# Performance work log

Hardware: AMD Instinct MI355X
Metric: run time of the kernel (lower is better)

Reference implementation:

```python
import jax, jax.numpy as jnp
import numpy as np

N_HEADS = 16
HEAD_DIM = 64
HIDDEN = N_HEADS * HEAD_DIM


def setup_inputs() -> dict:
    key = jax.random.key(0)
    ks = jax.random.split(key, 10)
    B, F, T = 2, 2048, 2048
    std = 0.02
    inp = {
        "from_tensor": jax.random.normal(ks[0], (B, F, HIDDEN), dtype=jnp.float32),
        "to_tensor": jax.random.normal(ks[1], (B, T, HIDDEN), dtype=jnp.float32),
        "attention_mask": jax.random.randint(ks[2], (B, F, T), 0, 2, dtype=jnp.int32),
        "Wq": jax.random.normal(ks[3], (HIDDEN, HIDDEN), dtype=jnp.float32) * std,
        "bq": jnp.zeros((HIDDEN,), dtype=jnp.float32),
        "Wk": jax.random.normal(ks[4], (HIDDEN, HIDDEN), dtype=jnp.float32) * std,
        "bk": jnp.zeros((HIDDEN,), dtype=jnp.float32),
        "Wv": jax.random.normal(ks[5], (HIDDEN, HIDDEN), dtype=jnp.float32) * std,
        "bv": jnp.zeros((HIDDEN,), dtype=jnp.float32),
    }
    return inp


def reference(from_tensor, to_tensor, attention_mask, Wq, bq, Wk, bk, Wv, bv):
    B, F, _ = from_tensor.shape
    T = to_tensor.shape[1]
    N, H = N_HEADS, HEAD_DIM

    # QKV projections (no activations: query/key/value act fns are None)
    q = (from_tensor @ Wq + bq).reshape(B, F, N, H)
    k = (to_tensor @ Wk + bk).reshape(B, T, N, H)
    v = (to_tensor @ Wv + bv).reshape(B, T, N, H)

    scores = jnp.einsum('BFNH,BTNH->BNFT', q, k) * (1.0 / np.sqrt(float(H)))
    # additive mask: mask [B,F,T] -> [B,1,F,T]; 0 entries get -10000
    adder = (1.0 - attention_mask.astype(jnp.float32))[:, None, :, :] * -10000.0
    scores = scores + adder
    probs = jax.nn.softmax(scores, axis=-1)  # dropout skipped (inference)

    context = jnp.einsum('BNFT,BTNH->BFNH', probs, v)
    return context.reshape(B, F, N * H)
```

## Files before the change

### kernel.cpp

```cpp
#include <hip/hip_runtime.h>


typedef short v8s __attribute__((ext_vector_type(8)));
typedef float v4f __attribute__((ext_vector_type(4)));
typedef unsigned short u16;
typedef unsigned int   u32;
typedef unsigned long long u64;

constexpr float QSCALE = 0.18033688011112042f;

__device__ __forceinline__ u16 f2bf(float f) {
    u32 u = __builtin_bit_cast(u32, f);
    u += 0x7fffu + ((u >> 16) & 1u);
    return (u16)(u >> 16);
}

__device__ __forceinline__ u32 pack_trunc(float a, float b) {
    return __builtin_amdgcn_perm(__builtin_bit_cast(u32, b),
                                 __builtin_bit_cast(u32, a), 0x07060302u);
}

__device__ __forceinline__ v8s ld8(const u16* p) {
    return *reinterpret_cast<const v8s*>(p);
}

__device__ __forceinline__ void async16(const void* g, void* l) {
    __builtin_amdgcn_global_load_lds(
        (const __attribute__((address_space(1))) u32*)g,
        (__attribute__((address_space(3))) u32*)l, 16, 0, 0);
}

__global__ __launch_bounds__(256) void prep(
    const float* __restrict__ from, const float* __restrict__ to,
    u16* __restrict__ Xf, u16* __restrict__ Xt,
    const float* __restrict__ Wq, const float* __restrict__ Wk, const float* __restrict__ Wv,
    u16* __restrict__ Wqt, u16* __restrict__ Wkt, u16* __restrict__ Wvt,
    const int* __restrict__ mask, u64* __restrict__ words) {
    __shared__ float tile[32][33];
    const int bid = blockIdx.x, tid = threadIdx.x;
    if (bid < 8192) {
        int i = bid * 256 + tid;
        const float4* s;
        ushort4* d;
        int j;
        if (i < 1048576) { s = (const float4*)from; d = (ushort4*)Xf; j = i; }
        else             { s = (const float4*)to;   d = (ushort4*)Xt; j = i - 1048576; }
        float4 v = s[j];
        ushort4 o;
        o.x = f2bf(v.x); o.y = f2bf(v.y); o.z = f2bf(v.z); o.w = f2bf(v.w);
        d[j] = o;
    } else if (bid < 11264) {
        const int r = bid - 8192;
        const int zz = r >> 10, rem = r & 1023;
        const float* W = zz == 0 ? Wq : (zz == 1 ? Wk : Wv);
        u16* Wt = zz == 0 ? Wqt : (zz == 1 ? Wkt : Wvt);
        const int tx = tid & 31, ty = tid >> 5;
        const int n0 = (rem & 31) * 32, k0 = (rem >> 5) * 32;
        for (int i = 0; i < 4; i++)
            tile[ty + i * 8][tx] = W[(size_t)(k0 + ty + i * 8) * 1024 + n0 + tx];
        __syncthreads();
        for (int i = 0; i < 4; i++)
            Wt[(size_t)(n0 + ty + i * 8) * 1024 + k0 + tx] = f2bf(tile[tx][ty + i * 8]);
    } else {
        int g = (bid - 11264) * 256 + tid;
        int w = g >> 6, lane = g & 63;
        int v = mask[(size_t)w * 64 + lane];
        u64 bits = __ballot(v != 0);
        if (lane == 0) words[w] = bits;
    }
}

__global__ __launch_bounds__(256) void gemm_qkv(
    const u16* __restrict__ Xf, const u16* __restrict__ Xt,
    const u16* __restrict__ Wqt, const u16* __restrict__ Wkt, const u16* __restrict__ Wvt,
    const float* __restrict__ bq, const float* __restrict__ bk, const float* __restrict__ bv,
    u16* __restrict__ Qb, u16* __restrict__ Kb, u16* __restrict__ Vtb) {
    const int z = blockIdx.z;
    const u16* A      = z == 0 ? Xf : Xt;
    const u16* Bt     = z == 0 ? Wqt : (z == 1 ? Wkt : Wvt);
    const float* bias = z == 0 ? bq : (z == 1 ? bk : bv);
    u16* C            = z == 0 ? Qb : (z == 1 ? Kb : Vtb);
    const int mode    = (z == 2);
    const float sc    = (z == 0) ? QSCALE : 1.0f;

    __shared__ u16 As[2][128][32];
    __shared__ u16 Bs[2][128][32];
    const uint4* Ag = reinterpret_cast<const uint4*>(A);
    const uint4* Bg = reinterpret_cast<const uint4*>(Bt);

    const int tid = threadIdx.x;
    const int lane = tid & 63, wave = tid >> 6;
    const int quad = lane >> 4, l16 = lane & 15;
    const int wm = wave >> 1, wn = wave & 1;
    const int m0 = blockIdx.x * 128, n0 = blockIdx.y * 128;

    const int cg  = (lane & 3) ^ ((lane >> 3) & 3);
    const int sw8 = (quad ^ ((l16 >> 1) & 3)) * 8;

    const int gi0 = wave * 4;
    const uint4 *ap0, *ap1, *ap2, *ap3, *bp0, *bp1, *bp2, *bp3;
    {
        const int rl = lane >> 2;
        const int rb0 = ((gi0 + 0) & 7) * 16 + rl, kh0 = (gi0 + 0) >> 3;
        const int rb1 = ((gi0 + 1) & 7) * 16 + rl, kh1 = (gi0 + 1) >> 3;
        const int rb2 = ((gi0 + 2) & 7) * 16 + rl, kh2 = (gi0 + 2) >> 3;
        const int rb3 = ((gi0 + 3) & 7) * 16 + rl, kh3 = (gi0 + 3) >> 3;
        ap0 = Ag + (size_t)(m0 + rb0) * 128 + kh0 * 4 + cg;
        ap1 = Ag + (size_t)(m0 + rb1) * 128 + kh1 * 4 + cg;
        ap2 = Ag + (size_t)(m0 + rb2) * 128 + kh2 * 4 + cg;
        ap3 = Ag + (size_t)(m0 + rb3) * 128 + kh3 * 4 + cg;
        bp0 = Bg + (size_t)(n0 + rb0) * 128 + kh0 * 4 + cg;
        bp1 = Bg + (size_t)(n0 + rb1) * 128 + kh1 * 4 + cg;
        bp2 = Bg + (size_t)(n0 + rb2) * 128 + kh2 * 4 + cg;
        bp3 = Bg + (size_t)(n0 + rb3) * 128 + kh3 * 4 + cg;
    }
    u16* Asl = (u16*)As + gi0 * 512;
    u16* Bsl = (u16*)Bs + gi0 * 512;

    v4f acc[4][4];
    for (int i = 0; i < 4; i++)
        for (int j = 0; j < 4; j++) acc[i][j] = (v4f)0.0f;

    for (int k0 = 0; k0 < 16; k0++) {
        __syncthreads();
        async16(ap0, Asl);        ap0 += 8;
        async16(ap1, Asl + 512);  ap1 += 8;
        async16(ap2, Asl + 1024); ap2 += 8;
        async16(ap3, Asl + 1536); ap3 += 8;
        async16(bp0, Bsl);        bp0 += 8;
        async16(bp1, Bsl + 512);  bp1 += 8;
        async16(bp2, Bsl + 1024); bp2 += 8;
        async16(bp3, Bsl + 1536); bp3 += 8;
        __syncthreads();

        #pragma unroll
        for (int kk = 0; kk < 2; kk++) {
            v8s af[4], bf[4];
            #pragma unroll
            for (int mt = 0; mt < 4; mt++) af[mt] = ld8(&As[kk][wm * 64 + mt * 16 + l16][sw8]);
            #pragma unroll
            for (int nt = 0; nt < 4; nt++) bf[nt] = ld8(&Bs[kk][wn * 64 + nt * 16 + l16][sw8]);
            #pragma unroll
            for (int mt = 0; mt < 4; mt++)
                #pragma unroll
                for (int nt = 0; nt < 4; nt++)
                    acc[mt][nt] = __builtin_amdgcn_mfma_f32_16x16x32_bf16(af[mt], bf[nt], acc[mt][nt], 0, 0, 0);
        }
    }

    #pragma unroll
    for (int nt = 0; nt < 4; nt++) {
        const int col = n0 + wn * 64 + nt * 16 + l16;
        const float bvv = bias[col];
        #pragma unroll
        for (int mt = 0; mt < 4; mt++) {
            const int mbase = m0 + wm * 64 + mt * 16 + quad * 4;
            if (mode == 0) {
                for (int r = 0; r < 4; r++)
                    C[(size_t)(mbase + r) * 1024 + col] = f2bf((acc[mt][nt][r] + bvv) * sc);
            } else {
                const int b = mbase >> 11, t = mbase & 2047;
                const int head = col >> 6, h = col & 63;
                ushort4 pk;
                pk.x = f2bf(acc[mt][nt][0] + bvv);
                pk.y = f2bf(acc[mt][nt][1] + bvv);
                pk.z = f2bf(acc[mt][nt][2] + bvv);
                pk.w = f2bf(acc[mt][nt][3] + bvv);
                *reinterpret_cast<ushort4*>(&C[(size_t)((b * 16 + head) * 64 + h) * 2048 + t]) = pk;
            }
        }
    }
}

__global__ __launch_bounds__(512, 4) void attn_fused(
    const u16* __restrict__ Qb, const u16* __restrict__ Kb,
    const u16* __restrict__ Vtb, const u64* __restrict__ mw,
    float* __restrict__ out) {
    __shared__ u16 Ks[2][2][64][32];
    __shared__ u16 Vs[2][2][64][32];
    __shared__ u32 Ps[8 * 1152];

    const int tid = threadIdx.x;
    const int lane = tid & 63, wave = tid >> 6;
    const int quad = lane >> 4, l16 = lane & 15;
    const int fwave = wave & 3, tw = wave >> 2;
    const int b = blockIdx.x >> 4, head = blockIdx.x & 15;
    const int f0 = blockIdx.y * 128;

    const uint4* Kg = reinterpret_cast<const uint4*>(Kb);
    const uint4* Vg = reinterpret_cast<const uint4*>(Vtb);
    const size_t vbase4 = (size_t)(b * 16 + head) * 64 * 256;

    const int cg  = (lane & 3) ^ ((lane >> 3) & 3);
    const int sw8 = (quad ^ ((l16 >> 1) & 3)) * 8;

    v8s qf[2][2];
    #pragma unroll
    for (int kk = 0; kk < 2; kk++)
        #pragma unroll
        for (int qh = 0; qh < 2; qh++)
            qf[kk][qh] = ld8(Qb + ((size_t)(b * 2048 + f0 + fwave * 32 + qh * 16 + l16) * 16 + head) * 64
                                + kk * 32 + quad * 8);

    v8s ones;
    #pragma unroll
    for (int i = 0; i < 8; i++) ones[i] = (short)0x3F80;

    const uint4 *sp0, *sp1, *sp2, *sp3;
    u16 *sd;
    size_t sinc;
    {
        const int rl = lane >> 2;
        if (wave < 4) {
            const int g0 = wave * 4;
            sd = (u16*)Ks + g0 * 512;
            sinc = 8192;
            #define KPTR(g) (Kg + ((size_t)(b * 2048 + ((g) >> 3) * 1024 + ((g) & 3) * 16 + rl) * 16 + head) * 8 \
                                + (((g) >> 2) & 1) * 4 + cg)
            sp0 = KPTR(g0); sp1 = KPTR(g0 + 1); sp2 = KPTR(g0 + 2); sp3 = KPTR(g0 + 3);
            #undef KPTR
        } else {
            const int g0 = (wave - 4) * 4;
            sd = (u16*)Vs + g0 * 512;
            sinc = 8;
            #define VPTR(g) (Vg + vbase4 + (size_t)(((g) & 3) * 16 + rl) * 256 + ((g) >> 3) * 128 \
                                + (((g) >> 2) & 1) * 4 + cg)
            sp0 = VPTR(g0); sp1 = VPTR(g0 + 1); sp2 = VPTR(g0 + 2); sp3 = VPTR(g0 + 3);
            #undef VPTR
        }
    }
    uint4* sd4 = reinterpret_cast<uint4*>(sd) + lane;

    v4f accO[2][4], accL[2];
    #pragma unroll
    for (int qh = 0; qh < 2; qh++) {
        accL[qh] = (v4f)0.0f;
        for (int ht = 0; ht < 4; ht++) accO[qh][ht] = (v4f)0.0f;
    }

    u32* myPs = Ps + wave * 1152;
    const u64* mrow = mw + (size_t)(b * 2048 + f0 + fwave * 32 + l16) * 32 + tw * 16;

    uint4 st0 = *sp0; sp0 += sinc;
    uint4 st1 = *sp1; sp1 += sinc;
    uint4 st2 = *sp2; sp2 += sinc;
    uint4 st3 = *sp3; sp3 += sinc;

    for (int it = 0; it < 16; it++) {
        __syncthreads();
        sd4[0]   = st0;
        sd4[64]  = st1;
        sd4[128] = st2;
        sd4[192] = st3;
        __syncthreads();

        if (it < 15) {
            st0 = *sp0; sp0 += sinc;
            st1 = *sp1; sp1 += sinc;
            st2 = *sp2; sp2 += sinc;
            st3 = *sp3; sp3 += sinc;
        }

        v4f s[2][4];
        #pragma unroll
        for (int qh = 0; qh < 2; qh++)
            for (int mt = 0; mt < 4; mt++) s[qh][mt] = (v4f)0.0f;
        #pragma unroll
        for (int kk = 0; kk < 2; kk++) {
            v8s kf[4];
            #pragma unroll
            for (int mt = 0; mt < 4; mt++) kf[mt] = ld8(&Ks[tw][kk][mt * 16 + l16][sw8]);
            #pragma unroll
            for (int qh = 0; qh < 2; qh++)
                #pragma unroll
                for (int mt = 0; mt < 4; mt++)
                    s[qh][mt] = __builtin_amdgcn_mfma_f32_16x16x32_bf16(kf[mt], qf[kk][qh], s[qh][mt], 0, 0, 0);
        }

        u32 pk[2][8];
        #pragma unroll
        for (int qh = 0; qh < 2; qh++) {
            const u64 w = mrow[qh * 512 + it];
            const u32 lo = (u32)(w >> (quad * 4));
            const u32 hi = (u32)(w >> (quad * 4 + 32));
            #pragma unroll
            for (int mt = 0; mt < 4; mt++) {
                const u32 bits = ((mt & 2) ? hi : lo) >> ((mt & 1) * 16);
                float p[4];
                #pragma unroll
                for (int r = 0; r < 4; r++) {
                    const float e = __builtin_amdgcn_exp2f(s[qh][mt][r]);
                    p[r] = ((bits >> r) & 1u) ? e : 0.0f;
                }
                pk[qh][mt * 2]     = pack_trunc(p[0], p[1]);
                pk[qh][mt * 2 + 1] = pack_trunc(p[2], p[3]);
            }
        }

        #pragma unroll
        for (int qh = 0; qh < 2; qh++) {
            const int row = qh * 16 + l16;
            #pragma unroll
            for (int mt = 0; mt < 4; mt++)
                *reinterpret_cast<uint2*>(&myPs[row * 36 + mt * 8 + quad * 2]) =
                    make_uint2(pk[qh][mt * 2], pk[qh][mt * 2 + 1]);
        }

        #pragma unroll
        for (int kk = 0; kk < 2; kk++) {
            v8s vf[4];
            #pragma unroll
            for (int ht = 0; ht < 4; ht++) vf[ht] = ld8(&Vs[tw][kk][ht * 16 + l16][sw8]);
            #pragma unroll
            for (int qh = 0; qh < 2; qh++) {
                const v8s pf = *reinterpret_cast<const v8s*>(
                    &myPs[(qh * 16 + l16) * 36 + kk * 16 + quad * 4]);
                #pragma unroll
                for (int ht = 0; ht < 4; ht++)
                    accO[qh][ht] = __builtin_amdgcn_mfma_f32_16x16x32_bf16(vf[ht], pf, accO[qh][ht], 0, 0, 0);
                accL[qh] = __builtin_amdgcn_mfma_f32_16x16x32_bf16(ones, pf, accL[qh], 0, 0, 0);
            }
        }
    }

    __syncthreads();
    float* fb = (float*)Ps;
    if (tw == 1) {
        float* wdst = fb + fwave * 2304 + lane * 36;
        #pragma unroll
        for (int qh = 0; qh < 2; qh++)
            #pragma unroll
            for (int ht = 0; ht < 4; ht++)
                *reinterpret_cast<v4f*>(wdst + (qh * 4 + ht) * 4) = accO[qh][ht];
        wdst[32] = accL[0][0];
        wdst[33] = accL[1][0];
    }
    __syncthreads();
    if (tw == 0) {
        const float* rsrc = fb + fwave * 2304 + lane * 36;
        float inv[2];
        #pragma unroll
        for (int qh = 0; qh < 2; qh++)
            inv[qh] = 1.0f / (accL[qh][0] + rsrc[32 + qh]);
        #pragma unroll
        for (int qh = 0; qh < 2; qh++) {
            const size_t ro = (size_t)(b * 2048 + f0 + fwave * 32 + qh * 16 + l16) * 1024 + head * 64;
            #pragma unroll
            for (int ht = 0; ht < 4; ht++) {
                const v4f p = *reinterpret_cast<const v4f*>(rsrc + (qh * 4 + ht) * 4);
                float4 o;
                o.x = (accO[qh][ht][0] + p[0]) * inv[qh];
                o.y = (accO[qh][ht][1] + p[1]) * inv[qh];
                o.z = (accO[qh][ht][2] + p[2]) * inv[qh];
                o.w = (accO[qh][ht][3] + p[3]) * inv[qh];
                *reinterpret_cast<float4*>(&out[ro + ht * 16 + quad * 4]) = o;
            }
        }
    }
}

extern "C" void kernel_launch(void* const* d_in, const int* in_sizes, int n_in,
                              void* d_out, int out_size, void* d_ws, size_t ws_size,
                              hipStream_t stream) {
    const float* from = (const float*)d_in[0];
    const float* to   = (const float*)d_in[1];
    const int*   mask = (const int*)d_in[2];
    const float* Wq = (const float*)d_in[3];
    const float* bq = (const float*)d_in[4];
    const float* Wk = (const float*)d_in[5];
    const float* bk = (const float*)d_in[6];
    const float* Wv = (const float*)d_in[7];
    const float* bv = (const float*)d_in[8];
    float* out = (float*)d_out;

    u16* Xf  = (u16*)d_ws;
    u16* Xt  = Xf  + 4194304;
    u16* Wqt = Xt  + 4194304;
    u16* Wkt = Wqt + 1048576;
    u16* Wvt = Wkt + 1048576;
    u16* Qb  = Wvt + 1048576;
    u16* Kb  = Qb  + 4194304;
    u16* Vtb = Kb  + 4194304;
    u64* mwords = (u64*)(Vtb + 4194304);

    prep<<<44032, 256, 0, stream>>>(from, to, Xf, Xt, Wq, Wk, Wv, Wqt, Wkt, Wvt, mask, mwords);

    gemm_qkv<<<dim3(32, 8, 3), 256, 0, stream>>>(Xf, Xt, Wqt, Wkt, Wvt, bq, bk, bv, Qb, Kb, Vtb);

    attn_fused<<<dim3(32, 16), 512, 0, stream>>>(Qb, Kb, Vtb, mwords, out);
}
```

Baseline: 221.0 us.

## Rework attention kernel to 32x32 MFMA with in-register P transpose and double-buffered KV

The attention kernel moves from 16x16x32 MFMA tiles to 32x32x16 tiles. The probability matrix now stays in registers and is rearranged with permlane32_swap, which removes the per-wave LDS round trip for P. The row sum is taken directly from the packed bf16 probabilities instead of a separate MFMA against a ones vector. K and V tiles are double-buffered in LDS with an XOR swizzle, leaving one barrier per iteration instead of two. The risks are the larger 32x32 accumulators raising register pressure at launch bounds (512,4), and the subtle permlane and mask-bit index mapping.

```diff
diff --git a/kernel.cpp b/kernel.cpp
--- a/kernel.cpp
+++ b/kernel.cpp
@@ -3,6 +3,8 @@
 
 typedef short v8s __attribute__((ext_vector_type(8)));
 typedef float v4f __attribute__((ext_vector_type(4)));
+typedef float v16f __attribute__((ext_vector_type(16)));
+typedef unsigned int v2u __attribute__((ext_vector_type(2)));
 typedef unsigned short u16;
 typedef unsigned int   u32;
 typedef unsigned long long u64;
@@ -176,186 +178,179 @@
     const u16* __restrict__ Qb, const u16* __restrict__ Kb,
     const u16* __restrict__ Vtb, const u64* __restrict__ mw,
     float* __restrict__ out) {
-    __shared__ u16 Ks[2][2][64][32];
-    __shared__ u16 Vs[2][2][64][32];
-    __shared__ u32 Ps[8 * 1152];
+    __shared__ u16 smem[2][2][128][64];
 
     const int tid = threadIdx.x;
     const int lane = tid & 63, wave = tid >> 6;
-    const int quad = lane >> 4, l16 = lane & 15;
+    const int l32 = lane & 31, hL = lane >> 5;
     const int fwave = wave & 3, tw = wave >> 2;
     const int b = blockIdx.x >> 4, head = blockIdx.x & 15;
     const int f0 = blockIdx.y * 128;
+    const int swz = (l32 & 7) << 3;
 
     const uint4* Kg = reinterpret_cast<const uint4*>(Kb);
     const uint4* Vg = reinterpret_cast<const uint4*>(Vtb);
     const size_t vbase4 = (size_t)(b * 16 + head) * 64 * 256;
 
-    const int cg  = (lane & 3) ^ ((lane >> 3) & 3);
-    const int sw8 = (quad ^ ((l16 >> 1) & 3)) * 8;
-
-    v8s qf[2][2];
-    #pragma unroll
-    for (int kk = 0; kk < 2; kk++)
-        #pragma unroll
-        for (int qh = 0; qh < 2; qh++)
-            qf[kk][qh] = ld8(Qb + ((size_t)(b * 2048 + f0 + fwave * 32 + qh * 16 + l16) * 16 + head) * 64
-                                + kk * 32 + quad * 8);
-
-    v8s ones;
-    #pragma unroll
-    for (int i = 0; i < 8; i++) ones[i] = (short)0x3F80;
+    v8s qf[4];
+    {
+        const u16* qp = Qb + ((size_t)(b * 2048 + f0 + fwave * 32 + l32) * 16 + head) * 64 + hL * 8;
+        #pragma unroll
+        for (int kk = 0; kk < 4; kk++) qf[kk] = ld8(qp + kk * 16);
+    }
 
     const uint4 *sp0, *sp1, *sp2, *sp3;
-    u16 *sd;
     size_t sinc;
+    u16* sdl;
     {
-        const int rl = lane >> 2;
+        const int rl8 = lane >> 3, cl8 = lane & 7;
+        sdl = (u16*)smem + (wave & 3) * 2048 + rl8 * 64 + ((cl8 ^ rl8) << 3)
+            + ((wave >= 4) ? 8192 : 0);
         if (wave < 4) {
-            const int g0 = wave * 4;
-            sd = (u16*)Ks + g0 * 512;
             sinc = 8192;
-            #define KPTR(g) (Kg + ((size_t)(b * 2048 + ((g) >> 3) * 1024 + ((g) & 3) * 16 + rl) * 16 + head) * 8 \
-                                + (((g) >> 2) & 1) * 4 + cg)
-            sp0 = KPTR(g0); sp1 = KPTR(g0 + 1); sp2 = KPTR(g0 + 2); sp3 = KPTR(g0 + 3);
-            #undef KPTR
+            #define KR(i) (wave * 32 + (i) * 8 + rl8)
+            #define KP(i) (Kg + ((size_t)(b * 2048 + (KR(i) >> 6) * 1024 + (KR(i) & 63)) * 16 + head) * 8 + cl8)
+            sp0 = KP(0); sp1 = KP(1); sp2 = KP(2); sp3 = KP(3);
+            #undef KP
+            #undef KR
         } else {
-            const int g0 = (wave - 4) * 4;
-            sd = (u16*)Vs + g0 * 512;
             sinc = 8;
-            #define VPTR(g) (Vg + vbase4 + (size_t)(((g) & 3) * 16 + rl) * 256 + ((g) >> 3) * 128 \
-                                + (((g) >> 2) & 1) * 4 + cg)
-            sp0 = VPTR(g0); sp1 = VPTR(g0 + 1); sp2 = VPTR(g0 + 2); sp3 = VPTR(g0 + 3);
-            #undef VPTR
-        }
-    }
-    uint4* sd4 = reinterpret_cast<uint4*>(sd) + lane;
-
-    v4f accO[2][4], accL[2];
-    #pragma unroll
-    for (int qh = 0; qh < 2; qh++) {
-        accL[qh] = (v4f)0.0f;
-        for (int ht = 0; ht < 4; ht++) accO[qh][ht] = (v4f)0.0f;
-    }
-
-    u32* myPs = Ps + wave * 1152;
-    const u64* mrow = mw + (size_t)(b * 2048 + f0 + fwave * 32 + l16) * 32 + tw * 16;
+            #define VR(i) ((wave - 4) * 32 + (i) * 8 + rl8)
+            #define VP(i) (Vg + vbase4 + (size_t)(VR(i) & 63) * 256 + (VR(i) >> 6) * 128 + cl8)
+            sp0 = VP(0); sp1 = VP(1); sp2 = VP(2); sp3 = VP(3);
+            #undef VP
+            #undef VR
+        }
+    }
+
+    v16f accO[2];
+    accO[0] = (v16f)0.0f;
+    accO[1] = (v16f)0.0f;
+    float lsA = 0.0f, lsB = 0.0f;
+
+    const u64* mrow = mw + (size_t)(b * 2048 + f0 + fwave * 32 + l32) * 32 + tw * 16;
 
     uint4 st0 = *sp0; sp0 += sinc;
     uint4 st1 = *sp1; sp1 += sinc;
     uint4 st2 = *sp2; sp2 += sinc;
     uint4 st3 = *sp3; sp3 += sinc;
+    *reinterpret_cast<uint4*>(sdl)        = st0;
+    *reinterpret_cast<uint4*>(sdl + 512)  = st1;
+    *reinterpret_cast<uint4*>(sdl + 1024) = st2;
+    *reinterpret_cast<uint4*>(sdl + 1536) = st3;
+    st0 = *sp0; sp0 += sinc;
+    st1 = *sp1; sp1 += sinc;
+    st2 = *sp2; sp2 += sinc;
+    st3 = *sp3; sp3 += sinc;
+    __syncthreads();
 
     for (int it = 0; it < 16; it++) {
+        const int buf = it & 1;
+        const u64 mword = mrow[it];
+
+        if (it < 15) {
+            u16* sdst = sdl + (buf ^ 1) * 16384;
+            *reinterpret_cast<uint4*>(sdst)        = st0;
+            *reinterpret_cast<uint4*>(sdst + 512)  = st1;
+            *reinterpret_cast<uint4*>(sdst + 1024) = st2;
+            *reinterpret_cast<uint4*>(sdst + 1536) = st3;
+            if (it < 14) {
+                st0 = *sp0; sp0 += sinc;
+                st1 = *sp1; sp1 += sinc;
+                st2 = *sp2; sp2 += sinc;
+                st3 = *sp3; sp3 += sinc;
+            }
+        }
+
+        const u16* kvb = (const u16*)smem + buf * 16384;
+
+        u32 pkw[2][8];
+        #pragma unroll
+        for (int mt = 0; mt < 2; mt++) {
+            v16f s = (v16f)0.0f;
+            #pragma unroll
+            for (int kk = 0; kk < 4; kk++) {
+                const v8s kf = *reinterpret_cast<const v8s*>(
+                    kvb + (tw * 64 + mt * 32 + l32) * 64 + ((kk * 16 + hL * 8) ^ swz));
+                s = __builtin_amdgcn_mfma_f32_32x32x16_bf16(kf, qf[kk], s, 0, 0, 0);
+            }
+            const u32 chunk = (u32)(mword >> (mt * 32 + hL * 4));
+            #pragma unroll
+            for (int wi = 0; wi < 8; wi++) {
+                const int r0 = wi * 2;
+                const int bp = (r0 & 3) + 8 * (r0 >> 2);
+                const float e0 = __builtin_amdgcn_exp2f(s[r0]);
+                const float e1 = __builtin_amdgcn_exp2f(s[r0 + 1]);
+                const float p0 = ((chunk >> bp) & 1u) ? e0 : 0.0f;
+                const float p1 = ((chunk >> (bp + 1)) & 1u) ? e1 : 0.0f;
+                const u32 w = pack_trunc(p0, p1);
+                pkw[mt][wi] = w;
+                lsA += __builtin_bit_cast(float, w << 16);
+                lsB += __builtin_bit_cast(float, w & 0xffff0000u);
+            }
+        }
+
+        #pragma unroll
+        for (int c = 0; c < 4; c++) {
+            const int mt = c >> 1, bse = (c & 1) * 4;
+            u32 pbw[4];
+            #pragma unroll
+            for (int u = 0; u < 2; u++) {
+                v2u rr = __builtin_amdgcn_permlane32_swap(
+                    pkw[mt][bse + u], pkw[mt][bse + 2 + u], false, false);
+                pbw[u]     = rr[0];
+                pbw[u + 2] = rr[1];
+            }
+            uint4 pq;
+            pq.x = pbw[0]; pq.y = pbw[1]; pq.z = pbw[2]; pq.w = pbw[3];
+            const v8s pb = __builtin_bit_cast(v8s, pq);
+            #pragma unroll
+            for (int ht = 0; ht < 2; ht++) {
+                const v8s vf = *reinterpret_cast<const v8s*>(
+                    kvb + 8192 + (tw * 64 + ht * 32 + l32) * 64 + ((c * 16 + hL * 8) ^ swz));
+                accO[ht] = __builtin_amdgcn_mfma_f32_32x32x16_bf16(vf, pb, accO[ht], 0, 0, 0);
+            }
+        }
+
         __syncthreads();
-        sd4[0]   = st0;
-        sd4[64]  = st1;
-        sd4[128] = st2;
-        sd4[192] = st3;
-        __syncthreads();
-
-        if (it < 15) {
-            st0 = *sp0; sp0 += sinc;
-            st1 = *sp1; sp1 += sinc;
-            st2 = *sp2; sp2 += sinc;
-            st3 = *sp3; sp3 += sinc;
-        }
-
-        v4f s[2][4];
-        #pragma unroll
-        for (int qh = 0; qh < 2; qh++)
-            for (int mt = 0; mt < 4; mt++) s[qh][mt] = (v4f)0.0f;
-        #pragma unroll
-        for (int kk = 0; kk < 2; kk++) {
-            v8s kf[4];
-            #pragma unroll
-            for (int mt = 0; mt < 4; mt++) kf[mt] = ld8(&Ks[tw][kk][mt * 16 + l16][sw8]);
-            #pragma unroll
-            for (int qh = 0; qh < 2; qh++)
-                #pragma unroll
-                for (int mt = 0; mt < 4; mt++)
-                    s[qh][mt] = __builtin_amdgcn_mfma_f32_16x16x32_bf16(kf[mt], qf[kk][qh], s[qh][mt], 0, 0, 0);
-        }
-
-        u32 pk[2][8];
-        #pragma unroll
-        for (int qh = 0; qh < 2; qh++) {
-            const u64 w = mrow[qh * 512 + it];
-            const u32 lo = (u32)(w >> (quad * 4));
-            const u32 hi = (u32)(w >> (quad * 4 + 32));
-            #pragma unroll
-            for (int mt = 0; mt < 4; mt++) {
-                const u32 bits = ((mt & 2) ? hi : lo) >> ((mt & 1) * 16);
-                float p[4];
-                #pragma unroll
-                for (int r = 0; r < 4; r++) {
-                    const float e = __builtin_amdgcn_exp2f(s[qh][mt][r]);
-                    p[r] = ((bits >> r) & 1u) ? e : 0.0f;
-                }
-                pk[qh][mt * 2]     = pack_trunc(p[0], p[1]);
-                pk[qh][mt * 2 + 1] = pack_trunc(p[2], p[3]);
-            }
-        }
-
-        #pragma unroll
-        for (int qh = 0; qh < 2; qh++) {
-            const int row = qh * 16 + l16;
-            #pragma unroll
-            for (int mt = 0; mt < 4; mt++)
-                *reinterpret_cast<uint2*>(&myPs[row * 36 + mt * 8 + quad * 2]) =
-                    make_uint2(pk[qh][mt * 2], pk[qh][mt * 2 + 1]);
-        }
-
-        #pragma unroll
-        for (int kk = 0; kk < 2; kk++) {
-            v8s vf[4];
-            #pragma unroll
-            for (int ht = 0; ht < 4; ht++) vf[ht] = ld8(&Vs[tw][kk][ht * 16 + l16][sw8]);
-            #pragma unroll
-            for (int qh = 0; qh < 2; qh++) {
-                const v8s pf = *reinterpret_cast<const v8s*>(
-                    &myPs[(qh * 16 + l16) * 36 + kk * 16 + quad * 4]);
-                #pragma unroll
-                for (int ht = 0; ht < 4; ht++)
-                    accO[qh][ht] = __builtin_amdgcn_mfma_f32_16x16x32_bf16(vf[ht], pf, accO[qh][ht], 0, 0, 0);
-                accL[qh] = __builtin_amdgcn_mfma_f32_16x16x32_bf16(ones, pf, accL[qh], 0, 0, 0);
-            }
-        }
-    }
-
-    __syncthreads();
-    float* fb = (float*)Ps;
+    }
+
+    const float lhalf = lsA + lsB;
+    const float lsum = lhalf + __shfl_xor(lhalf, 32);
+
+    float* fb = (float*)smem;
     if (tw == 1) {
         float* wdst = fb + fwave * 2304 + lane * 36;
         #pragma unroll
-        for (int qh = 0; qh < 2; qh++)
-            #pragma unroll
-            for (int ht = 0; ht < 4; ht++)
-                *reinterpret_cast<v4f*>(wdst + (qh * 4 + ht) * 4) = accO[qh][ht];
-        wdst[32] = accL[0][0];
-        wdst[33] = accL[1][0];
+        for (int ht = 0; ht < 2; ht++)
+            #pragma unroll
+            for (int g = 0; g < 4; g++) {
+                v4f t;
+                t[0] = accO[ht][g * 4 + 0];
+                t[1] = accO[ht][g * 4 + 1];
+                t[2] = accO[ht][g * 4 + 2];
+                t[3] = accO[ht][g * 4 + 3];
+                *reinterpret_cast<v4f*>(wdst + ht * 16 + g * 4) = t;
+            }
+        wdst[32] = lsum;
     }
     __syncthreads();
     if (tw == 0) {
         const float* rsrc = fb + fwave * 2304 + lane * 36;
-        float inv[2];
-        #pragma unroll
-        for (int qh = 0; qh < 2; qh++)
-            inv[qh] = 1.0f / (accL[qh][0] + rsrc[32 + qh]);
-        #pragma unroll
-        for (int qh = 0; qh < 2; qh++) {
-            const size_t ro = (size_t)(b * 2048 + f0 + fwave * 32 + qh * 16 + l16) * 1024 + head * 64;
-            #pragma unroll
-            for (int ht = 0; ht < 4; ht++) {
-                const v4f p = *reinterpret_cast<const v4f*>(rsrc + (qh * 4 + ht) * 4);
+        const float inv = 1.0f / (lsum + rsrc[32]);
+        const size_t ro = (size_t)(b * 2048 + f0 + fwave * 32 + l32) * 1024 + head * 64;
+        #pragma unroll
+        for (int ht = 0; ht < 2; ht++)
+            #pragma unroll
+            for (int g = 0; g < 4; g++) {
+                const v4f p = *reinterpret_cast<const v4f*>(rsrc + ht * 16 + g * 4);
                 float4 o;
-                o.x = (accO[qh][ht][0] + p[0]) * inv[qh];
-                o.y = (accO[qh][ht][1] + p[1]) * inv[qh];
-                o.z = (accO[qh][ht][2] + p[2]) * inv[qh];
-                o.w = (accO[qh][ht][3] + p[3]) * inv[qh];
-                *reinterpret_cast<float4*>(&out[ro + ht * 16 + quad * 4]) = o;
-            }
-        }
+                o.x = (accO[ht][g * 4 + 0] + p[0]) * inv;
+                o.y = (accO[ht][g * 4 + 1] + p[1]) * inv;
+                o.z = (accO[ht][g * 4 + 2] + p[2]) * inv;
+                o.w = (accO[ht][g * 4 + 3] + p[3]) * inv;
+                *reinterpret_cast<float4*>(&out[ro + ht * 32 + g * 8 + hL * 4]) = o;
+            }
     }
 }
 
```

New measurement: 223.5 us. No clear change (+1.1%).
